# Kernel optimization log

Measured on AMD Instinct MI355X. Metric: run time of the kernel, lower is better.

Reference implementation:

```python
import jax, jax.numpy as jnp
import numpy as np

EPS = 1e-5
K_NUM, EDGE_TYPE = 5, 2  # k_num = A_fixed_partitions(3) + edge_type(2)


def _bn(x, gamma, beta):
    # training-mode BatchNorm2d: batch stats over (N, T, V) per channel
    m = jnp.mean(x, axis=(0, 2, 3), keepdims=True)
    v = jnp.var(x, axis=(0, 2, 3), keepdims=True)
    return (x - m) * jax.lax.rsqrt(v + EPS) * gamma[None, :, None, None] + beta[None, :, None, None]


def setup_inputs() -> dict:
    key = jax.random.key(0)
    ks = jax.random.split(key, 6)
    N, C, T, V = 32, 64, 300, 25
    Cout, Kt = 64, 9
    x = jax.random.normal(ks[0], (N, C, T, V), jnp.float32)
    A = jax.random.uniform(ks[1], (K_NUM - EDGE_TYPE, V, V), jnp.float32) / V  # fixed adjacency (already scaled by edge_importance)
    B = jax.random.uniform(ks[2], (N, EDGE_TYPE, V, V), jnp.float32) / V      # per-sample adaptive adjacency A_act
    lamda_act = jnp.full((1,), 0.5, jnp.float32)
    conv_w = jax.random.normal(ks[3], (Cout * K_NUM, C), jnp.float32) * (1.0 / np.sqrt(C))  # 1x1 conv weight
    conv_b = jnp.zeros((Cout * K_NUM,), jnp.float32)
    bn1_g = jnp.ones((Cout,), jnp.float32)
    bn1_b = jnp.zeros((Cout,), jnp.float32)
    tcn_w = jax.random.normal(ks[4], (Cout, Cout, Kt, 1), jnp.float32) * (1.0 / np.sqrt(Cout * Kt))
    tcn_b = jnp.zeros((Cout,), jnp.float32)
    bn2_g = jnp.ones((Cout,), jnp.float32)
    bn2_b = jnp.zeros((Cout,), jnp.float32)
    return dict(x=x, A=A, B=B, lamda_act=lamda_act, conv_w=conv_w, conv_b=conv_b,
                bn1_g=bn1_g, bn1_b=bn1_b, tcn_w=tcn_w, tcn_b=tcn_b, bn2_g=bn2_g, bn2_b=bn2_b)


def reference(x, A, B, lamda_act, conv_w, conv_b, bn1_g, bn1_b, tcn_w, tcn_b, bn2_g, bn2_b):
    n, c, t, v = x.shape
    res = x  # identity residual (in_ch == out_ch, stride 1)
    # SpatialGcn: 1x1 conv (pure channel GEMM) -> split -> dual einsum graph conv
    y = jnp.einsum('nctv,oc->notv', x, conv_w) + conv_b[None, :, None, None]  # (n, K*Cout, t, v)
    cout = y.shape[1] // K_NUM
    y = y.reshape(n, K_NUM, cout, t, v)
    x1 = jnp.einsum('nkctv,kvw->nctw', y[:, :K_NUM - EDGE_TYPE], A)   # fixed adjacency
    x2 = jnp.einsum('nkctv,nkvw->nctw', y[:, K_NUM - EDGE_TYPE:], B)  # adaptive adjacency
    g = x1 + x2 * lamda_act[0]
    # tcn: BN -> ReLU -> temporal conv (9,1) pad (4,0) -> BN -> Dropout(0)=identity
    h = jax.nn.relu(_bn(g, bn1_g, bn1_b))
    h = jax.lax.conv_general_dilated(h, tcn_w, window_strides=(1, 1),
                                     padding=((4, 4), (0, 0)),
                                     dimension_numbers=('NCHW', 'OIHW', 'NCHW'))
    h = h + tcn_b[None, :, None, None]
    h = _bn(h, bn2_g, bn2_b)
    return jax.nn.relu(h + res)
```

## Files before the change

### kernel.cpp

```cpp
#include <hip/hip_runtime.h>
#include <hip/hip_bf16.h>

#define N_  32
#define C_  64
#define T_  300
#define V_  25
#define TV  (T_*V_)
#define CTV (C_*TV)
#define NELEM (N_*CTV)
#define CNTF 240000.0f

typedef float f32x4 __attribute__((ext_vector_type(4)));
typedef short bf16x8 __attribute__((ext_vector_type(8)));
typedef short s4v __attribute__((ext_vector_type(4)));
typedef short s8v __attribute__((ext_vector_type(8)));

__device__ __forceinline__ unsigned short f2bf(float f) {
    unsigned u = __float_as_uint(f);
    unsigned r = u + 0x7fffu + ((u >> 16) & 1u);
    return (unsigned short)(r >> 16);
}
__device__ __forceinline__ float bf2f(unsigned short u) {
    return __uint_as_float(((unsigned)u) << 16);
}

__global__ __launch_bounds__(256) void k_prep(
    const float* __restrict__ conv_w, const float* __restrict__ tw,
    unsigned short* __restrict__ w2b, unsigned short* __restrict__ twb)
{
    int tid = blockIdx.x*256 + threadIdx.x;
    for (int e = tid; e < 20480; e += 8192) {
        int ks = e >> 11, c = (e >> 5) & 63, kk = e & 31;
        w2b[e] = f2bf(conv_w[(((ks>>1)*64 + c)*64) + (ks&1)*32 + kk]);
    }
    for (int e = tid; e < 36864; e += 8192) {
        int gi = e >> 11, c = (e >> 5) & 63, kk = e & 31;
        int dt = gi >> 1, ks = gi & 1;
        twb[e] = f2bf(tw[(c*64 + 32*ks + kk)*9 + dt]);
    }
}

__global__ __launch_bounds__(256) void k_gcn(
    const float* __restrict__ x, const float* __restrict__ A,
    const float* __restrict__ B, const float* __restrict__ lamda,
    const unsigned short* __restrict__ w2b, const float* __restrict__ conv_b,
    unsigned short* __restrict__ gout, float* __restrict__ stats3)
{
    __shared__ unsigned short ash[5*32*40];
    __shared__ unsigned short zsh[32*328];
    __shared__ unsigned short gsh[25*68];
    __shared__ float csum[160];
    __shared__ float sbc[320];

    const int tb = blockIdx.x, n = blockIdx.y;
    const int t0 = tb*10;
    const int tid = threadIdx.x;
    const int lane = tid & 63, wv = tid >> 6;
    const int lg = lane >> 4, lr = lane & 15;
    const int crow = lr + 16*wv;
    const int cbase = 16*wv + 4*lg;

    bf16x8 wfrag[10];
    #pragma unroll
    for (int ks = 0; ks < 10; ++ks)
        wfrag[ks] = *(const bf16x8*)&w2b[(ks*64 + crow)*32 + 8*lg];

    const float lam = lamda[0];
    for (int e = tid; e < 6400; e += 256) {
        int k = e / 1280, r = e % 1280, w = r / 40, v = r % 40;
        float val = 0.f;
        if (w < 25 && v < 25)
            val = (k < 3) ? A[k*625 + v*25 + w]
                          : lam * B[((n<<1) + (k-3))*625 + v*25 + w];
        ash[e] = f2bf(val);
    }
    for (int e = tid; e < 320; e += 256) sbc[e] = conv_b[e];
    __syncthreads();
    for (int e = tid; e < 160; e += 256) {
        int k = e / 32, w = e % 32;
        float s = 0.f;
        for (int v = 0; v < 25; ++v) s += bf2f(ash[k*1280 + w*40 + v]);
        csum[e] = s;
    }
    __syncthreads();

    float bs0[4], bs1[4];
    #pragma unroll
    for (int r = 0; r < 4; ++r) {
        float s0 = 0.f, s1 = 0.f;
        #pragma unroll
        for (int k = 0; k < 5; ++k) {
            float cb = sbc[k*64 + cbase + r];
            s0 += cb * csum[k*32 + lr];
            s1 += cb * csum[k*32 + lr + 16];
        }
        bs0[r] = s0; bs1[r] = s1;
    }

    float sacc[4] = {0,0,0,0}, qacc[4] = {0,0,0,0};

    const float* xrow = x + n*CTV + crow*TV + t0*V_;
    float xf[8];
    #pragma unroll
    for (int i = 0; i < 8; ++i) { int v = 8*lg + i; xf[i] = (v < 25) ? xrow[v] : 0.f; }

    for (int tl = 0; tl < 10; ++tl) {
        bf16x8 xfrag;
        #pragma unroll
        for (int i = 0; i < 8; ++i) xfrag[i] = (short)f2bf(xf[i]);
        if (tl < 9) {
            const float* xn = xrow + (tl+1)*V_;
            #pragma unroll
            for (int i = 0; i < 8; ++i) { int v = 8*lg + i; xf[i] = (v < 25) ? xn[v] : 0.f; }
        }
        #pragma unroll
        for (int k = 0; k < 5; ++k)
        #pragma unroll
        for (int nt = 0; nt < 2; ++nt) {
            bf16x8 bfrag = *(const bf16x8*)&ash[k*1280 + (lr + 16*nt)*40 + 8*lg];
            f32x4 z = {0.f,0.f,0.f,0.f};
            z = __builtin_amdgcn_mfma_f32_16x16x32_bf16(xfrag, bfrag, z, 0, 0, 0);
            s4v z4;
            #pragma unroll
            for (int r = 0; r < 4; ++r) z4[r] = (short)f2bf(z[r]);
            *(s4v*)&zsh[(lr + 16*nt)*328 + k*64 + 16*wv + 4*lg] = z4;
        }
        __syncthreads();
        f32x4 acc0 = {0.f,0.f,0.f,0.f}, acc1 = {0.f,0.f,0.f,0.f};
        #pragma unroll
        for (int ks = 0; ks < 10; ++ks) {
            bf16x8 b0 = *(const bf16x8*)&zsh[lr*328 + 32*ks + 8*lg];
            bf16x8 b1 = *(const bf16x8*)&zsh[(lr+16)*328 + 32*ks + 8*lg];
            acc0 = __builtin_amdgcn_mfma_f32_16x16x32_bf16(wfrag[ks], b0, acc0, 0, 0, 0);
            acc1 = __builtin_amdgcn_mfma_f32_16x16x32_bf16(wfrag[ks], b1, acc1, 0, 0, 0);
        }
        s4v g0, g1;
        #pragma unroll
        for (int r = 0; r < 4; ++r) {
            float v0 = acc0[r] + bs0[r];
            float v1 = acc1[r] + bs1[r];
            g0[r] = (short)f2bf(v0); g1[r] = (short)f2bf(v1);
            sacc[r] += v0 + (lr < 9 ? v1 : 0.f);
            qacc[r] += v0*v0 + (lr < 9 ? v1*v1 : 0.f);
        }
        *(s4v*)&gsh[lr*68 + cbase] = g0;
        if (lr < 9) *(s4v*)&gsh[(lr+16)*68 + cbase] = g1;
        __syncthreads();
        unsigned short* grow = gout + (size_t)(n*300 + t0 + tl)*1600;
        for (int e = tid; e < 1600; e += 256)
            grow[e] = gsh[(e >> 6)*68 + (e & 63)];
    }

    #pragma unroll
    for (int r = 0; r < 4; ++r) {
        float s = sacc[r], q = qacc[r];
        s += __shfl_xor(s, 1); s += __shfl_xor(s, 2);
        s += __shfl_xor(s, 4); s += __shfl_xor(s, 8);
        q += __shfl_xor(q, 1); q += __shfl_xor(q, 2);
        q += __shfl_xor(q, 4); q += __shfl_xor(q, 8);
        if (lr == 0) {
            stats3[(n*30 + tb)*128 + cbase + r] = s;
            stats3[(n*30 + tb)*128 + 64 + cbase + r] = q;
        }
    }
}

__global__ __launch_bounds__(256) void k_fin(
    const float* __restrict__ src, int count, float* __restrict__ sbo,
    const float* __restrict__ gma, const float* __restrict__ bta)
{
    const int c = blockIdx.x, tid = threadIdx.x;
    float s = 0.f, q = 0.f;
    for (int b = tid; b < count; b += 256) {
        s += src[b*128 + c];
        q += src[b*128 + 64 + c];
    }
    #pragma unroll
    for (int m = 1; m < 64; m <<= 1) { s += __shfl_xor(s, m); q += __shfl_xor(q, m); }
    __shared__ float rs[4], rq[4];
    if ((tid & 63) == 0) { rs[tid>>6] = s; rq[tid>>6] = q; }
    __syncthreads();
    if (tid == 0) {
        s = rs[0]+rs[1]+rs[2]+rs[3]; q = rq[0]+rq[1]+rq[2]+rq[3];
        float mean = s / CNTF, var = q / CNTF - mean*mean;
        float sc = gma[c] * rsqrtf(var + 1e-5f);
        sbo[c] = sc;
        sbo[64 + c] = bta[c] - mean*sc;
    }
}

__global__ __launch_bounds__(256) void k_tcn(
    const unsigned short* __restrict__ gin, const float* __restrict__ sb,
    const unsigned short* __restrict__ twb, const float* __restrict__ tb,
    unsigned short* __restrict__ hout, float* __restrict__ stats4)
{
    __shared__ unsigned short pT[400*40];
    __shared__ float sbs[128];

    const int n = blockIdx.y, tt = blockIdx.x, t0 = tt*8;
    const int tid = threadIdx.x;
    const int lane = tid & 63, wv = tid >> 6;
    const int lg = lane >> 4, lr = lane & 15;
    const int c = lr + 16*wv;
    const int cbase = 16*wv + 4*lg;

    bf16x8 af[18];
    #pragma unroll
    for (int gi = 0; gi < 18; ++gi)
        af[gi] = *(const bf16x8*)&twb[(gi*64 + c)*32 + 8*lg];

    for (int e = tid; e < 128; e += 256) sbs[e] = sb[e];

    f32x4 acc[13];
    #pragma unroll
    for (int nt = 0; nt < 13; ++nt) acc[nt] = (f32x4){0.f,0.f,0.f,0.f};

    for (int ks = 0; ks < 2; ++ks) {
        __syncthreads();
        for (int e8 = tid; e8 < 1600; e8 += 256) {
            int tl = e8 / 100, r = e8 % 100, w = r >> 2, ch = r & 3;
            int tg = t0 - 4 + tl;
            int i8 = 32*ks + ch*8;
            s8v val8 = {0,0,0,0,0,0,0,0};
            if (tg >= 0 && tg < 300) {
                s8v raw = *(const s8v*)&gin[(size_t)((n*300 + tg)*25 + w)*64 + i8];
                #pragma unroll
                for (int j = 0; j < 8; ++j) {
                    float f = fmaf(bf2f((unsigned short)raw[j]), sbs[i8+j], sbs[64+i8+j]);
                    val8[j] = (short)f2bf(fmaxf(f, 0.f));
                }
            }
            *(s8v*)&pT[(tl*25 + w)*40 + ch*8] = val8;
        }
        __syncthreads();

        #pragma unroll
        for (int nt = 0; nt < 13; ++nt) {
            int col = lr + 16*nt; if (col > 199) col = 199;
            #pragma unroll
            for (int dt = 0; dt < 9; ++dt) {
                bf16x8 b = *(const bf16x8*)&pT[(col + 25*dt)*40 + 8*lg];
                acc[nt] = __builtin_amdgcn_mfma_f32_16x16x32_bf16(af[dt*2 + ks], b, acc[nt], 0, 0, 0);
            }
        }
    }

    const int lim = min(200, (300 - t0)*25);
    float tbc[4];
    #pragma unroll
    for (int r = 0; r < 4; ++r) tbc[r] = tb[cbase + r];

    float sacc[4] = {0,0,0,0}, qacc[4] = {0,0,0,0};
    #pragma unroll
    for (int nt = 0; nt < 13; ++nt) {
        int col = lr + 16*nt;
        if (col < lim) {
            #pragma unroll
            for (int r = 0; r < 4; ++r) {
                float v = acc[nt][r] + tbc[r];
                sacc[r] += v; qacc[r] += v*v;
            }
        }
    }
    #pragma unroll
    for (int r = 0; r < 4; ++r) {
        float s = sacc[r], q = qacc[r];
        s += __shfl_xor(s, 1); s += __shfl_xor(s, 2);
        s += __shfl_xor(s, 4); s += __shfl_xor(s, 8);
        q += __shfl_xor(q, 1); q += __shfl_xor(q, 2);
        q += __shfl_xor(q, 4); q += __shfl_xor(q, 8);
        if (lr == 0) {
            stats4[(n*38 + tt)*128 + cbase + r] = s;
            stats4[(n*38 + tt)*128 + 64 + cbase + r] = q;
        }
    }

    __syncthreads();
    unsigned short* hbuf = pT;
    #pragma unroll
    for (int nt = 0; nt < 13; ++nt) {
        int col = lr + 16*nt;
        if (col < 200) {
            #pragma unroll
            for (int r = 0; r < 4; ++r)
                hbuf[(cbase + r)*200 + col] = f2bf(acc[nt][r] + tbc[r]);
        }
    }
    __syncthreads();
    for (int e = tid; e < 3200; e += 256) {
        int row = e / 50, c4 = (e % 50)*4;
        if (c4 < lim) {
            s4v o = *(const s4v*)&hbuf[row*200 + c4];
            *(s4v*)&hout[((size_t)(n*64 + row)*300 + t0)*25 + c4] = o;
        }
    }
}

__global__ __launch_bounds__(256) void k_out(
    const unsigned short* __restrict__ h, const float* __restrict__ x,
    const float* __restrict__ sb, float* __restrict__ out)
{
    int i4 = blockIdx.x * 256 + threadIdx.x;
    if (i4 >= NELEM/4) return;
    int c = ((i4*4) / TV) & 63;
    float s2 = sb[128 + c], b2 = sb[192 + c];
    s4v hv = *(const s4v*)&h[i4*4];
    float4 xv = ((const float4*)x)[i4];
    float4 o;
    o.x = fmaxf(fmaf(bf2f((unsigned short)hv[0]), s2, b2) + xv.x, 0.f);
    o.y = fmaxf(fmaf(bf2f((unsigned short)hv[1]), s2, b2) + xv.y, 0.f);
    o.z = fmaxf(fmaf(bf2f((unsigned short)hv[2]), s2, b2) + xv.z, 0.f);
    o.w = fmaxf(fmaf(bf2f((unsigned short)hv[3]), s2, b2) + xv.w, 0.f);
    ((float4*)out)[i4] = o;
}

extern "C" void kernel_launch(void* const* d_in, const int* in_sizes, int n_in,
                              void* d_out, int out_size, void* d_ws, size_t ws_size,
                              hipStream_t stream)
{
    const float* x      = (const float*)d_in[0];
    const float* A      = (const float*)d_in[1];
    const float* B      = (const float*)d_in[2];
    const float* lamda  = (const float*)d_in[3];
    const float* conv_w = (const float*)d_in[4];
    const float* conv_b = (const float*)d_in[5];
    const float* bn1_g  = (const float*)d_in[6];
    const float* bn1_b  = (const float*)d_in[7];
    const float* tcn_w  = (const float*)d_in[8];
    const float* tcn_b  = (const float*)d_in[9];
    const float* bn2_g  = (const float*)d_in[10];
    const float* bn2_b  = (const float*)d_in[11];

    unsigned short* g = (unsigned short*)d_ws;
    unsigned short* h = g + NELEM;
    float* stats3 = (float*)(h + NELEM);
    float* stats4 = stats3 + 960*128;
    float* sb     = stats4 + 1216*128;
    unsigned short* w2b = (unsigned short*)(sb + 256);
    unsigned short* twb = w2b + 20480;

    k_prep<<<32, 256, 0, stream>>>(conv_w, tcn_w, w2b, twb);
    k_gcn<<<dim3(30, N_), 256, 0, stream>>>(x, A, B, lamda, w2b, conv_b, g, stats3);
    k_fin<<<64, 256, 0, stream>>>(stats3, 960, sb, bn1_g, bn1_b);
    k_tcn<<<dim3(38, N_), 256, 0, stream>>>(g, sb, twb, tcn_b, h, stats4);
    k_fin<<<64, 256, 0, stream>>>(stats4, 1216, sb + 128, bn2_g, bn2_b);
    k_out<<<NELEM/4/256, 256, 0, stream>>>(h, x, sb, (float*)d_out);
}
```

Measured before the change: 144.4 us.

## Split k_tcn column tiles across 8 waves to cut per-thread registers

The temporal conv kernel goes from 4 to 8 waves per block. Each pair of waves now shares a 16-channel tile and splits the 13 column tiles (7 each), and the weight fragments are loaded per K-half (9 instead of 18). This shrinks per-thread accumulator and weight registers to raise occupancy and latency hiding. In exchange the weight fragments are reloaded per K-step, the stats buffer doubles with per-half partials, and the 8th wave's tiles are mostly clamped redundant work (14 tiles computed vs 13).

```diff
diff --git a/kernel.cpp b/kernel.cpp
--- a/kernel.cpp
+++ b/kernel.cpp
@@ -189,7 +189,7 @@
     }
 }
 
-__global__ __launch_bounds__(256) void k_tcn(
+__global__ __launch_bounds__(512, 4) void k_tcn(
     const unsigned short* __restrict__ gin, const float* __restrict__ sb,
     const unsigned short* __restrict__ twb, const float* __restrict__ tb,
     unsigned short* __restrict__ hout, float* __restrict__ stats4)
@@ -201,26 +201,27 @@
     const int tid = threadIdx.x;
     const int lane = tid & 63, wv = tid >> 6;
     const int lg = lane >> 4, lr = lane & 15;
-    const int c = lr + 16*wv;
-    const int cbase = 16*wv + 4*lg;
-
-    bf16x8 af[18];
-    #pragma unroll
-    for (int gi = 0; gi < 18; ++gi)
-        af[gi] = *(const bf16x8*)&twb[(gi*64 + c)*32 + 8*lg];
-
-    for (int e = tid; e < 128; e += 256) sbs[e] = sb[e];
-
-    f32x4 acc[13];
-    #pragma unroll
-    for (int nt = 0; nt < 13; ++nt) acc[nt] = (f32x4){0.f,0.f,0.f,0.f};
+    const int ct = wv & 3, ch = wv >> 2;
+    const int cfrag = ct*16 + lr;
+    const int cbase = ct*16 + 4*lg;
+
+    for (int e = tid; e < 128; e += 512) sbs[e] = sb[e];
+
+    f32x4 acc[7];
+    #pragma unroll
+    for (int i = 0; i < 7; ++i) acc[i] = (f32x4){0.f,0.f,0.f,0.f};
 
     for (int ks = 0; ks < 2; ++ks) {
+        bf16x8 af[9];
+        #pragma unroll
+        for (int dt = 0; dt < 9; ++dt)
+            af[dt] = *(const bf16x8*)&twb[((dt*2 + ks)*64 + cfrag)*32 + 8*lg];
+
         __syncthreads();
-        for (int e8 = tid; e8 < 1600; e8 += 256) {
-            int tl = e8 / 100, r = e8 % 100, w = r >> 2, ch = r & 3;
+        for (int e8 = tid; e8 < 1600; e8 += 512) {
+            int tl = e8 / 100, r = e8 % 100, w = r >> 2, c8 = r & 3;
             int tg = t0 - 4 + tl;
-            int i8 = 32*ks + ch*8;
+            int i8 = 32*ks + c8*8;
             s8v val8 = {0,0,0,0,0,0,0,0};
             if (tg >= 0 && tg < 300) {
                 s8v raw = *(const s8v*)&gin[(size_t)((n*300 + tg)*25 + w)*64 + i8];
@@ -230,17 +231,17 @@
                     val8[j] = (short)f2bf(fmaxf(f, 0.f));
                 }
             }
-            *(s8v*)&pT[(tl*25 + w)*40 + ch*8] = val8;
+            *(s8v*)&pT[(tl*25 + w)*40 + c8*8] = val8;
         }
         __syncthreads();
 
         #pragma unroll
-        for (int nt = 0; nt < 13; ++nt) {
-            int col = lr + 16*nt; if (col > 199) col = 199;
+        for (int i = 0; i < 7; ++i) {
+            int col = lr + 16*(ch*7 + i); if (col > 199) col = 199;
             #pragma unroll
             for (int dt = 0; dt < 9; ++dt) {
                 bf16x8 b = *(const bf16x8*)&pT[(col + 25*dt)*40 + 8*lg];
-                acc[nt] = __builtin_amdgcn_mfma_f32_16x16x32_bf16(af[dt*2 + ks], b, acc[nt], 0, 0, 0);
+                acc[i] = __builtin_amdgcn_mfma_f32_16x16x32_bf16(af[dt], b, acc[i], 0, 0, 0);
             }
         }
     }
@@ -252,12 +253,12 @@
 
     float sacc[4] = {0,0,0,0}, qacc[4] = {0,0,0,0};
     #pragma unroll
-    for (int nt = 0; nt < 13; ++nt) {
-        int col = lr + 16*nt;
+    for (int i = 0; i < 7; ++i) {
+        int col = lr + 16*(ch*7 + i);
         if (col < lim) {
             #pragma unroll
             for (int r = 0; r < 4; ++r) {
-                float v = acc[nt][r] + tbc[r];
+                float v = acc[i][r] + tbc[r];
                 sacc[r] += v; qacc[r] += v*v;
             }
         }
@@ -270,24 +271,25 @@
         q += __shfl_xor(q, 1); q += __shfl_xor(q, 2);
         q += __shfl_xor(q, 4); q += __shfl_xor(q, 8);
         if (lr == 0) {
-            stats4[(n*38 + tt)*128 + cbase + r] = s;
-            stats4[(n*38 + tt)*128 + 64 + cbase + r] = q;
+            float* dst = stats4 + (size_t)((n*38 + tt)*2 + ch)*128;
+            dst[cbase + r] = s;
+            dst[64 + cbase + r] = q;
         }
     }
 
     __syncthreads();
     unsigned short* hbuf = pT;
     #pragma unroll
-    for (int nt = 0; nt < 13; ++nt) {
-        int col = lr + 16*nt;
+    for (int i = 0; i < 7; ++i) {
+        int col = lr + 16*(ch*7 + i);
         if (col < 200) {
             #pragma unroll
             for (int r = 0; r < 4; ++r)
-                hbuf[(cbase + r)*200 + col] = f2bf(acc[nt][r] + tbc[r]);
-        }
-    }
-    __syncthreads();
-    for (int e = tid; e < 3200; e += 256) {
+                hbuf[(cbase + r)*200 + col] = f2bf(acc[i][r] + tbc[r]);
+        }
+    }
+    __syncthreads();
+    for (int e = tid; e < 3200; e += 512) {
         int row = e / 50, c4 = (e % 50)*4;
         if (c4 < lim) {
             s4v o = *(const s4v*)&hbuf[row*200 + c4];
@@ -335,14 +337,14 @@
     unsigned short* h = g + NELEM;
     float* stats3 = (float*)(h + NELEM);
     float* stats4 = stats3 + 960*128;
-    float* sb     = stats4 + 1216*128;
+    float* sb     = stats4 + 2432*128;
     unsigned short* w2b = (unsigned short*)(sb + 256);
     unsigned short* twb = w2b + 20480;
 
     k_prep<<<32, 256, 0, stream>>>(conv_w, tcn_w, w2b, twb);
     k_gcn<<<dim3(30, N_), 256, 0, stream>>>(x, A, B, lamda, w2b, conv_b, g, stats3);
     k_fin<<<64, 256, 0, stream>>>(stats3, 960, sb, bn1_g, bn1_b);
-    k_tcn<<<dim3(38, N_), 256, 0, stream>>>(g, sb, twb, tcn_b, h, stats4);
-    k_fin<<<64, 256, 0, stream>>>(stats4, 1216, sb + 128, bn2_g, bn2_b);
+    k_tcn<<<dim3(38, N_), 512, 0, stream>>>(g, sb, twb, tcn_b, h, stats4);
+    k_fin<<<64, 256, 0, stream>>>(stats4, 2432, sb + 128, bn2_g, bn2_b);
     k_out<<<NELEM/4/256, 256, 0, stream>>>(h, x, sb, (float*)d_out);
 }
```

After: 138.2 us. 1.05x faster.
